# Optimization experiments

Hardware: AMD Instinct MI355X
Metric: run time of the kernel (lower is better)

The kernel has to match this reference:

```python
import jax, jax.numpy as jnp
import numpy as np

WS = 7  # window_size
EPS = 1e-5


def _ln(x, w, b):
    mu = jnp.mean(x, axis=-1, keepdims=True)
    var = jnp.mean((x - mu) ** 2, axis=-1, keepdims=True)
    return (x - mu) / jnp.sqrt(var + EPS) * w + b


def _mamba(xw, A, Bm, Cm):
    # xw: (N, T, C). h_t = x_t @ B + h_{t-1} @ A ; out = h @ C
    xB = xw @ Bm                      # (N, T, C) precompute input projection
    xs = jnp.swapaxes(xB, 0, 1)       # (T, N, C)

    def step(h, xb):
        h = xb + h @ A
        return h, h

    h0 = jnp.zeros_like(xs[0])
    _, hs = jax.lax.scan(step, h0, xs)  # (T, N, C)
    h = jnp.swapaxes(hs, 0, 1)          # (N, T, C)
    return h @ Cm


def setup_inputs() -> dict:
    key = jax.random.key(0)
    ks = jax.random.split(key, 12)
    dim = 384
    hid = 4 * dim
    s = 1.0 / np.sqrt(dim)
    d = {}
    d["x"] = jax.random.normal(ks[0], (16, 56, 56, dim), jnp.float32)
    # recurrence matrices scaled for numerical stability over T=49 steps
    d["A"] = jax.random.normal(ks[1], (dim, dim), jnp.float32) * (1.0 / dim)
    d["Bm"] = jax.random.normal(ks[2], (dim, dim), jnp.float32) * s
    d["Cm"] = jax.random.normal(ks[3], (dim, dim), jnp.float32) * s
    d["ln1_w"] = jnp.ones((dim,), jnp.float32)
    d["ln1_b"] = jnp.zeros((dim,), jnp.float32)
    d["ln2_w"] = jnp.ones((dim,), jnp.float32)
    d["ln2_b"] = jnp.zeros((dim,), jnp.float32)
    d["W1"] = jax.random.normal(ks[4], (dim, hid), jnp.float32) * s
    d["b1"] = jnp.zeros((hid,), jnp.float32)
    d["W2"] = jax.random.normal(ks[5], (hid, dim), jnp.float32) * (1.0 / np.sqrt(hid))
    d["b2"] = jnp.zeros((dim,), jnp.float32)
    return d


def reference(x, A, Bm, Cm, ln1_w, ln1_b, ln2_w, ln2_b, W1, b1, W2, b2):
    Bn, H, W, C = x.shape
    ws = WS
    # window_partition: (B,H,W,C) -> (B*nH*nW, ws*ws, C)
    w = x.reshape(Bn, H // ws, ws, W // ws, ws, C)
    w = w.transpose(0, 1, 3, 2, 4, 5).reshape(-1, ws * ws, C)
    w = _ln(w, ln1_w, ln1_b)
    w = _mamba(w, A, Bm, Cm)
    # window_reverse
    xr = w.reshape(Bn, H // ws, W // ws, ws, ws, C)
    xr = xr.transpose(0, 1, 3, 2, 4, 5).reshape(Bn, H, W, C)
    # MLP with residual (exact GELU, matching torch default)
    y = _ln(xr, ln2_w, ln2_b)
    y = jax.nn.gelu(y @ W1 + b1, approximate=False) @ W2 + b2
    return xr + y
```

## Files before the change

### kernel.cpp

```cpp
#include <hip/hip_runtime.h>
#include <hip/hip_bf16.h>
#include <math.h>

#define CDIM 384
#define HIDDIM 1536
#define HW56 56
#define WS 7
#define T49 49
#define MTOK 50176
#define MH 25088
#define DPOW 5
#define KSCAN (DPOW * CDIM)

typedef __bf16 bf16x8 __attribute__((ext_vector_type(8)));
typedef __bf16 bf16x4 __attribute__((ext_vector_type(4)));
typedef __bf16 bf16x2 __attribute__((ext_vector_type(2)));
typedef float f32x4 __attribute__((ext_vector_type(4)));

typedef const __attribute__((address_space(1))) void gas_void;
typedef __attribute__((address_space(3))) void las_void;

__device__ __forceinline__ void async16(const void* g, void* l) {
    __builtin_amdgcn_global_load_lds((gas_void*)g, (las_void*)l, 16, 0, 0);
}

__device__ __forceinline__ float fast_rcp(float x) {
#if __has_builtin(__builtin_amdgcn_rcpf)
    return __builtin_amdgcn_rcpf(x);
#else
    return 1.f / x;
#endif
}

__device__ __forceinline__ float fast_gelu(float v) {
    const float t = v + 0.044715f * v * v * v;
    const float e = __expf(-1.5957691216057308f * t);
    return v * fast_rcp(1.f + e);
}



__global__ __launch_bounds__(256) void transpose_to_bf16(
    const float* __restrict__ src, __bf16* __restrict__ dst, int R, int C)
{
    __shared__ float tile[64][65];
    const int c0 = blockIdx.x * 64, r0 = blockIdx.y * 64;
#pragma unroll
    for (int p = 0; p < 16; p++) {
        const int idx = threadIdx.x + p * 256;
        const int rr = idx >> 6, cc = idx & 63;
        tile[cc][rr] = src[(size_t)(r0 + rr) * C + c0 + cc];
    }
    __syncthreads();
#pragma unroll
    for (int p = 0; p < 16; p++) {
        const int idx = threadIdx.x + p * 256;
        const int cc = idx >> 6, rr = idx & 63;
        dst[(size_t)(c0 + cc) * R + r0 + rr] = (__bf16)tile[cc][rr];
    }
}

struct GemmJob  { const float* A; const float* B; float* D; };
struct GemmJobs { GemmJob j[3]; };

__global__ __launch_bounds__(256) void multi_gemm(GemmJobs jobs)
{
    __shared__ float As[16][68];
    __shared__ float Bs[16][68];
    const int tx = threadIdx.x & 15, ty = threadIdx.x >> 4;
    const int m0 = blockIdx.x * 64, n0 = blockIdx.y * 64;
    const GemmJob job = jobs.j[blockIdx.z];
    const float* Ain = job.A;
    const float* Bmat = job.B;
    float acc[4][4] = {};

    for (int k0 = 0; k0 < CDIM; k0 += 16) {
#pragma unroll
        for (int l = 0; l < 4; l++) {
            const int idx = threadIdx.x + l * 256;
            const int am = idx >> 4, ak = idx & 15;
            As[ak][am] = Ain[(size_t)(m0 + am) * CDIM + (k0 + ak)];
            const int bk = idx >> 6, bn = idx & 63;
            Bs[bk][bn] = Bmat[(size_t)(k0 + bk) * CDIM + (n0 + bn)];
        }
        __syncthreads();
#pragma unroll
        for (int kk = 0; kk < 16; kk++) {
            const float4 a4 = *reinterpret_cast<const float4*>(&As[kk][ty * 4]);
            const float4 b4 = *reinterpret_cast<const float4*>(&Bs[kk][tx * 4]);
            const float a[4]  = {a4.x, a4.y, a4.z, a4.w};
            const float bv[4] = {b4.x, b4.y, b4.z, b4.w};
#pragma unroll
            for (int i = 0; i < 4; i++)
#pragma unroll
                for (int j = 0; j < 4; j++) acc[i][j] += a[i] * bv[j];
        }
        __syncthreads();
    }
#pragma unroll
    for (int i = 0; i < 4; i++)
#pragma unroll
        for (int j = 0; j < 4; j++)
            job.D[(size_t)(m0 + ty * 4 + i) * CDIM + n0 + tx * 4 + j] = acc[i][j];
}

__global__ __launch_bounds__(256) void mcat_gemm(
    const float* __restrict__ Am, const float* __restrict__ Bmat, __bf16* __restrict__ Out)
{
    __shared__ float As[16][68];
    __shared__ float Bs[16][68];
    const int tx = threadIdx.x & 15, ty = threadIdx.x >> 4;
    const int m0 = blockIdx.x * 64, n0 = blockIdx.y * 64;
    const float* Ain = Am + (size_t)blockIdx.z * (CDIM * CDIM);
    float acc[4][4] = {};

    for (int k0 = 0; k0 < CDIM; k0 += 16) {
#pragma unroll
        for (int l = 0; l < 4; l++) {
            const int idx = threadIdx.x + l * 256;
            const int am = idx >> 4, ak = idx & 15;
            As[ak][am] = Ain[(size_t)(m0 + am) * CDIM + (k0 + ak)];
            const int bk = idx >> 6, bn = idx & 63;
            Bs[bk][bn] = Bmat[(size_t)(k0 + bk) * CDIM + (n0 + bn)];
        }
        __syncthreads();
#pragma unroll
        for (int kk = 0; kk < 16; kk++) {
            const float4 a4 = *reinterpret_cast<const float4*>(&As[kk][ty * 4]);
            const float4 b4 = *reinterpret_cast<const float4*>(&Bs[kk][tx * 4]);
            const float a[4]  = {a4.x, a4.y, a4.z, a4.w};
            const float bv[4] = {b4.x, b4.y, b4.z, b4.w};
#pragma unroll
            for (int i = 0; i < 4; i++)
#pragma unroll
                for (int j = 0; j < 4; j++) acc[i][j] += a[i] * bv[j];
        }
        __syncthreads();
    }
#pragma unroll
    for (int i = 0; i < 4; i++)
#pragma unroll
        for (int j = 0; j < 4; j++) {
            const int n = n0 + tx * 4 + j, m = m0 + ty * 4 + i;
            Out[(size_t)n * KSCAN + blockIdx.z * CDIM + m] = (__bf16)acc[i][j];
        }
}

__global__ void zerofill(float* p) { p[threadIdx.x] = 0.f; }

__global__ __launch_bounds__(256) void ln1_win_kernel(
    const float* __restrict__ x,
    const float* __restrict__ w,
    const float* __restrict__ b,
    __bf16* __restrict__ out)
{
    const int row  = blockIdx.x * 4 + (threadIdx.x >> 6);
    const int lane = threadIdx.x & 63;
    const int n = row / T49, t = row - n * T49;
    const int bb = n >> 6, rem = n & 63, hw = rem >> 3, ww = rem & 7;
    const int pi = t / WS, pj = t - pi * WS;
    const size_t pix = (size_t)(bb * HW56 + hw * WS + pi) * HW56 + (ww * WS + pj);
    const float* xr = x + pix * CDIM;

    float2 v[3]; float s = 0.f;
#pragma unroll
    for (int k = 0; k < 3; k++) {
        v[k] = *(const float2*)&xr[lane * 2 + 128 * k];
        s += v[k].x + v[k].y;
    }
#pragma unroll
    for (int off = 32; off > 0; off >>= 1) s += __shfl_down(s, off);
    const float mu = __shfl(s, 0) * (1.f / CDIM);
    float vs = 0.f;
#pragma unroll
    for (int k = 0; k < 3; k++) {
        const float dx = v[k].x - mu, dy = v[k].y - mu;
        vs += dx * dx + dy * dy;
    }
#pragma unroll
    for (int off = 32; off > 0; off >>= 1) vs += __shfl_down(vs, off);
    const float rstd = rsqrtf(__shfl(vs, 0) * (1.f / CDIM) + 1e-5f);

    __bf16* o = out + (size_t)row * CDIM;
#pragma unroll
    for (int k = 0; k < 3; k++) {
        const int c = lane * 2 + 128 * k;
        const float2 wv = *(const float2*)&w[c];
        const float2 bv = *(const float2*)&b[c];
        bf16x2 o2;
        o2[0] = (__bf16)((v[k].x - mu) * rstd * wv.x + bv.x);
        o2[1] = (__bf16)((v[k].y - mu) * rstd * wv.y + bv.y);
        *(bf16x2*)&o[c] = o2;
    }
}

__global__ __launch_bounds__(256) void ln2_kernel(
    const float* __restrict__ xr,
    const float* __restrict__ w,
    const float* __restrict__ b,
    __bf16* __restrict__ out)
{
    const int row  = blockIdx.x * 4 + (threadIdx.x >> 6);
    const int lane = threadIdx.x & 63;
    const float* xrow = xr + (size_t)row * CDIM;
    float2 v[3]; float s = 0.f;
#pragma unroll
    for (int k = 0; k < 3; k++) {
        v[k] = *(const float2*)&xrow[lane * 2 + 128 * k];
        s += v[k].x + v[k].y;
    }
#pragma unroll
    for (int off = 32; off > 0; off >>= 1) s += __shfl_down(s, off);
    const float mu = __shfl(s, 0) * (1.f / CDIM);
    float vs = 0.f;
#pragma unroll
    for (int k = 0; k < 3; k++) {
        const float dx = v[k].x - mu, dy = v[k].y - mu;
        vs += dx * dx + dy * dy;
    }
#pragma unroll
    for (int off = 32; off > 0; off >>= 1) vs += __shfl_down(vs, off);
    const float rstd = rsqrtf(__shfl(vs, 0) * (1.f / CDIM) + 1e-5f);

    __bf16* o = out + (size_t)row * CDIM;
#pragma unroll
    for (int k = 0; k < 3; k++) {
        const int c = lane * 2 + 128 * k;
        const float2 wv = *(const float2*)&w[c];
        const float2 bv = *(const float2*)&b[c];
        bf16x2 o2;
        o2[0] = (__bf16)((v[k].x - mu) * rstd * wv.x + bv.x);
        o2[1] = (__bf16)((v[k].y - mu) * rstd * wv.y + bv.y);
        *(bf16x2*)&o[c] = o2;
    }
}

__global__ __launch_bounds__(256) void gemm_scan(
    const __bf16* __restrict__ X,
    const __bf16* __restrict__ Wt,
    const __bf16* __restrict__ zerob,
    float* __restrict__ Out)
{
    __shared__ __bf16 Xs[136 * 64];
    __shared__ __bf16 Ws[128 * 64];

    const int nwg = gridDim.x;
    const int q8 = nwg >> 3, r8 = nwg & 7;
    const int xcd = blockIdx.x & 7, lin = blockIdx.x >> 3;
    const int id = (xcd < r8 ? xcd * (q8 + 1) : r8 * (q8 + 1) + (xcd - r8) * q8) + lin;
    const int bx = id / 3, by = id - bx * 3;

    const int tid  = threadIdx.x;
    const int w    = tid >> 6;
    const int lane = tid & 63;
    const int quad = lane >> 4, l15 = lane & 15;
    const int wm = w & 1, wn = w >> 1;
    const int m0 = bx * 128;
    const int n0 = by * 128;
    const int srow8 = lane >> 3;
    const int scol  = ((lane & 7) ^ srow8) * 8;

    const bool head  = (m0 == 0);
    const bool tailb = (m0 + 132 > MTOK);

    int tpos[4];
#pragma unroll
    for (int s = 0; s < 4; s++) tpos[s] = (m0 + wm * 64 + s * 16 + l15) % T49;

    const __bf16* Wbase = Wt + (size_t)(n0 + w * 32 + srow8) * KSCAN + scol;
    const __bf16* Xbase = X + ((size_t)m0 + w * 32 + srow8) * CDIM + scol - 4 * CDIM;

    const bf16x8 zero8 = {};
    f32x4 acc[4][4] = {};

    for (int kb = 0; kb < CDIM; kb += 64) {
        for (int j = 0; j < DPOW; j++) {
            __syncthreads();
            if (j == 0) {
#pragma unroll
                for (int c = 0; c < 4; c++) {
                    const __bf16* src = Xbase + (size_t)(c * 8) * CDIM + kb;
                    if (head && w == 0 && c == 0 && srow8 < 4) src = zerob;
                    async16(src, &Xs[(w * 32 + c * 8) * 64]);
                }
                if (w == 0) {
                    const int tk = m0 + 124 + srow8;
                    const __bf16* src = X + (size_t)tk * CDIM + kb + scol;
                    if (tailb && tk >= MTOK) src = zerob;
                    async16(src, &Xs[128 * 64]);
                }
            }
#pragma unroll
            for (int c = 0; c < 4; c++) {
                async16(Wbase + (size_t)(c * 8) * KSCAN + j * CDIM + kb, &Ws[(w * 32 + c * 8) * 64]);
            }
            __syncthreads();
#pragma unroll
            for (int kh = 0; kh < 2; kh++) {
                bf16x8 a[4], b[4];
#pragma unroll
                for (int s = 0; s < 4; s++) {
                    const int xrow = wm * 64 + s * 16 + l15 + 4 - j;
                    const int apos = ((kh * 4 + quad) ^ (xrow & 7)) * 8;
                    const bf16x8 av = *(const bf16x8*)&Xs[xrow * 64 + apos];
                    a[s] = (tpos[s] >= j) ? av : zero8;
                    const int rb = wn * 64 + s * 16 + l15;
                    const int bpos = ((kh * 4 + quad) ^ (l15 & 7)) * 8;
                    b[s] = *(const bf16x8*)&Ws[rb * 64 + bpos];
                }
#pragma unroll
                for (int i = 0; i < 4; i++)
#pragma unroll
                    for (int jj = 0; jj < 4; jj++)
                        acc[i][jj] = __builtin_amdgcn_mfma_f32_16x16x32_bf16(b[jj], a[i], acc[i][jj], 0, 0, 0);
            }
        }
    }

#pragma unroll
    for (int i = 0; i < 4; i++) {
        const int gm = m0 + wm * 64 + i * 16 + l15;
        const int n = gm / T49, t = gm - n * T49;
        const int bb = n >> 6, rem = n & 63, hw = rem >> 3, ww = rem & 7;
        const int pi = t / WS, pj = t - pi * WS;
        const size_t orow = (size_t)(bb * HW56 + hw * WS + pi) * HW56 + (ww * WS + pj);
#pragma unroll
        for (int jj = 0; jj < 4; jj++) {
            const int gn0 = n0 + wn * 64 + jj * 16 + quad * 4;
            *(f32x4*)&Out[orow * CDIM + gn0] = acc[i][jj];
        }
    }
}

template <int EPI, int NY>
__global__ __launch_bounds__(256) void gemm_mfma(
    const __bf16* __restrict__ X,
    const __bf16* __restrict__ Wt,
    const float*  __restrict__ bias,
    const float*  resid,
    void* Out, const int K, const int Nout)
{
    __shared__ __bf16 Xs[2][128 * 64];
    __shared__ __bf16 Ws[2][128 * 64];

    const int nwg = gridDim.x;
    const int q8 = nwg >> 3, r8 = nwg & 7;
    const int xcd = blockIdx.x & 7, lin = blockIdx.x >> 3;
    const int id = (xcd < r8 ? xcd * (q8 + 1) : r8 * (q8 + 1) + (xcd - r8) * q8) + lin;
    const int bx = id / NY, by = id - bx * NY;

    const int tid  = threadIdx.x;
    const int w    = tid >> 6;
    const int lane = tid & 63;
    const int quad = lane >> 4, l15 = lane & 15;
    const int wm = w & 1, wn = w >> 1;
    const size_t m0 = (size_t)bx * 128;
    const int n0 = by * 128;
    const int srow = w * 32 + (lane >> 3);
    const int scol = (((lane & 7) ^ (lane >> 3)) * 8);

    f32x4 acc[4][4] = {};

    const __bf16* Xrow = X + (m0 + srow) * (size_t)K + scol;
    const __bf16* Wrow = Wt + ((size_t)(n0 + srow)) * K + scol;

    auto stage = [&](int p, int bufi) {
        const int k0 = p * 64;
#pragma unroll
        for (int c = 0; c < 4; c++) {
            async16(Xrow + (size_t)(c * 8) * K + k0, &Xs[bufi][(w * 32 + c * 8) * 64]);
            async16(Wrow + (size_t)(c * 8) * K + k0, &Ws[bufi][(w * 32 + c * 8) * 64]);
        }
    };

    const int NP = K >> 6;
    stage(0, 0);
    __syncthreads();

    for (int p = 0; p < NP; p++) {
        if (p + 1 < NP) stage(p + 1, (p + 1) & 1);
        const int cb = p & 1;
#pragma unroll
        for (int kk = 0; kk < 2; kk++) {
            bf16x8 a[4], b[4];
#pragma unroll
            for (int s = 0; s < 4; s++) {
                const int ra = wm * 64 + s * 16 + l15;
                const int rb = wn * 64 + s * 16 + l15;
                const int pos = ((kk * 4 + quad) ^ (l15 & 7)) * 8;
                a[s] = *(const bf16x8*)&Xs[cb][ra * 64 + pos];
                b[s] = *(const bf16x8*)&Ws[cb][rb * 64 + pos];
            }
#pragma unroll
            for (int i = 0; i < 4; i++)
#pragma unroll
                for (int j = 0; j < 4; j++)
                    acc[i][j] = __builtin_amdgcn_mfma_f32_16x16x32_bf16(b[j], a[i], acc[i][j], 0, 0, 0);
        }
        __syncthreads();
    }

#pragma unroll
    for (int i = 0; i < 4; i++) {
        const size_t gm = m0 + wm * 64 + i * 16 + l15;
#pragma unroll
        for (int j = 0; j < 4; j++) {
            const int gn0 = n0 + wn * 64 + j * 16 + quad * 4;
            const float4 bs = *(const float4*)&bias[gn0];
            if (EPI == 2) {
                bf16x4 h;
#pragma unroll
                for (int r = 0; r < 4; r++) {
                    const float v = acc[i][j][r] + (&bs.x)[r];
                    h[r] = (__bf16)fast_gelu(v);
                }
                *(bf16x4*)&((__bf16*)Out)[gm * (size_t)Nout + gn0] = h;
            } else {
                const float4 rs = *(const float4*)&resid[gm * CDIM + gn0];
                f32x4 o;
#pragma unroll
                for (int r = 0; r < 4; r++) o[r] = acc[i][j][r] + (&bs.x)[r] + (&rs.x)[r];
                *(f32x4*)&((float*)Out)[gm * CDIM + gn0] = o;
            }
        }
    }
}

extern "C" void kernel_launch(void* const* d_in, const int* in_sizes, int n_in,
                              void* d_out, int out_size, void* d_ws, size_t ws_size,
                              hipStream_t stream) {
    const float* x    = (const float*)d_in[0];
    const float* A    = (const float*)d_in[1];
    const float* Bm   = (const float*)d_in[2];
    const float* Cm   = (const float*)d_in[3];
    const float* ln1w = (const float*)d_in[4];
    const float* ln1b = (const float*)d_in[5];
    const float* ln2w = (const float*)d_in[6];
    const float* ln2b = (const float*)d_in[7];
    const float* W1   = (const float*)d_in[8];
    const float* b1   = (const float*)d_in[9];
    const float* W2   = (const float*)d_in[10];
    const float* b2   = (const float*)d_in[11];

    float* outf = (float*)d_out;

    char* ws = (char*)d_ws;
    __bf16* B1     = (__bf16*)ws;
    float*  P      = (float*) (ws + 38535168);
    float*  A2     = (float*) (ws + 38535168 + DPOW * 589824);
    __bf16* Mcat_t = (__bf16*)(ws + 38535168 + (DPOW + 1) * 589824);
    float*  zerob  = (float*) (ws + 38535168 + (DPOW + 1) * 589824 + KSCAN * 768);
    float*  A4     = (float*) (ws + 38535168 + (DPOW + 1) * 589824 + KSCAN * 768 + 4096);
    __bf16* Hid    = (__bf16*)ws;
    __bf16* B2     = (__bf16*)(ws + 77070336);
    __bf16* W1_t   = (__bf16*)(ws + 115605504);
    __bf16* W2_t   = (__bf16*)(ws + 116785152);

    hipMemcpyAsync(P, Bm, (size_t)CDIM * CDIM * 4, hipMemcpyDeviceToDevice, stream);
    zerofill<<<1, 128, 0, stream>>>(zerob);
    transpose_to_bf16<<<dim3(24, 6), 256, 0, stream>>>(W1, W1_t, 384, 1536);
    transpose_to_bf16<<<dim3(6, 24), 256, 0, stream>>>(W2, W2_t, 1536, 384);

    {
        GemmJobs j1;
        j1.j[0] = {A, A, A2};
        j1.j[1] = {Bm, A, P + 1 * CDIM * CDIM};
        j1.j[2] = {A, A, A2};
        multi_gemm<<<dim3(6, 6, 2), 256, 0, stream>>>(j1);
        GemmJobs j2;
        j2.j[0] = {A2, A2, A4};
        j2.j[1] = {P, A2, P + 2 * CDIM * CDIM};
        j2.j[2] = {P + 1 * CDIM * CDIM, A2, P + 3 * CDIM * CDIM};
        multi_gemm<<<dim3(6, 6, 3), 256, 0, stream>>>(j2);
        GemmJobs j3;
        j3.j[0] = {P, A4, P + 4 * CDIM * CDIM};
        j3.j[1] = j3.j[0];
        j3.j[2] = j3.j[0];
        multi_gemm<<<dim3(6, 6, 1), 256, 0, stream>>>(j3);
    }
    mcat_gemm<<<dim3(6, 6, DPOW), 256, 0, stream>>>(P, Cm, Mcat_t);

    ln1_win_kernel<<<MTOK / 4, 256, 0, stream>>>(x, ln1w, ln1b, B1);
    gemm_scan<<<dim3((MTOK / 128) * 3), 256, 0, stream>>>(B1, Mcat_t, (const __bf16*)zerob, outf);
    ln2_kernel<<<MTOK / 4, 256, 0, stream>>>(outf, ln2w, ln2b, B2);
    for (int h = 0; h < 2; h++) {
        const size_t off = (size_t)h * MH * CDIM;
        gemm_mfma<2, 12><<<dim3((MH / 128) * 12), 256, 0, stream>>>(B2 + off, W1_t, b1, nullptr, Hid, 384, 1536);
        gemm_mfma<3, 3><<<dim3((MH / 128) * 3), 256, 0, stream>>>(Hid, W2_t, b2, outf + off, outf + off, 1536, 384);
    }
}
```

Before: 587.2 us.

## Reassociate weight-power precompute and shrink MLP GEMM K-stage to 32

The small weight-precompute chain is reassociated: instead of computing A^4 and then Bm*A^4 before multiplying by Cm, it computes U2=A^2*Cm and forms the fifth block as P2*U2. This drops the memcpy and one serial multi_gemm launch, and mcat_gemm now takes per-slice A/B pointers. Separately, the MLP MFMA GEMM stages 32-wide K tiles instead of 64, with a new LDS swizzle. That halves shared memory per block to help occupancy, at the cost of twice as many pipeline iterations and barriers.

```diff
diff --git a/kernel.cpp b/kernel.cpp
--- a/kernel.cpp
+++ b/kernel.cpp
@@ -104,14 +104,16 @@
             job.D[(size_t)(m0 + ty * 4 + i) * CDIM + n0 + tx * 4 + j] = acc[i][j];
 }
 
-__global__ __launch_bounds__(256) void mcat_gemm(
-    const float* __restrict__ Am, const float* __restrict__ Bmat, __bf16* __restrict__ Out)
+struct McatJobs { const float* Aj[DPOW]; const float* Bj[DPOW]; };
+
+__global__ __launch_bounds__(256) void mcat_gemm(McatJobs jobs, __bf16* __restrict__ Out)
 {
     __shared__ float As[16][68];
     __shared__ float Bs[16][68];
     const int tx = threadIdx.x & 15, ty = threadIdx.x >> 4;
     const int m0 = blockIdx.x * 64, n0 = blockIdx.y * 64;
-    const float* Ain = Am + (size_t)blockIdx.z * (CDIM * CDIM);
+    const float* Ain  = jobs.Aj[blockIdx.z];
+    const float* Bmat = jobs.Bj[blockIdx.z];
     float acc[4][4] = {};
 
     for (int k0 = 0; k0 < CDIM; k0 += 16) {
@@ -340,8 +342,8 @@
     const float*  resid,
     void* Out, const int K, const int Nout)
 {
-    __shared__ __bf16 Xs[2][128 * 64];
-    __shared__ __bf16 Ws[2][128 * 64];
+    __shared__ __bf16 Xs[2][128 * 32];
+    __shared__ __bf16 Ws[2][128 * 32];
 
     const int nwg = gridDim.x;
     const int q8 = nwg >> 3, r8 = nwg & 7;
@@ -356,47 +358,44 @@
     const int wm = w & 1, wn = w >> 1;
     const size_t m0 = (size_t)bx * 128;
     const int n0 = by * 128;
-    const int srow = w * 32 + (lane >> 3);
-    const int scol = (((lane & 7) ^ (lane >> 3)) * 8);
+    const int srow4 = lane >> 2;
+    const int sc4   = lane & 3;
 
     f32x4 acc[4][4] = {};
 
-    const __bf16* Xrow = X + (m0 + srow) * (size_t)K + scol;
-    const __bf16* Wrow = Wt + ((size_t)(n0 + srow)) * K + scol;
-
     auto stage = [&](int p, int bufi) {
-        const int k0 = p * 64;
-#pragma unroll
-        for (int c = 0; c < 4; c++) {
-            async16(Xrow + (size_t)(c * 8) * K + k0, &Xs[bufi][(w * 32 + c * 8) * 64]);
-            async16(Wrow + (size_t)(c * 8) * K + k0, &Ws[bufi][(w * 32 + c * 8) * 64]);
+        const int k0 = p * 32;
+#pragma unroll
+        for (int c = 0; c < 2; c++) {
+            const int R  = w * 32 + c * 16 + srow4;
+            const int lc = ((sc4 ^ ((R >> 1) & 3)) * 8);
+            async16(X  + (m0 + R) * (size_t)K + k0 + lc, &Xs[bufi][(w * 32 + c * 16) * 32]);
+            async16(Wt + (size_t)(n0 + R) * K + k0 + lc, &Ws[bufi][(w * 32 + c * 16) * 32]);
         }
     };
 
-    const int NP = K >> 6;
+    const int NP = K >> 5;
     stage(0, 0);
     __syncthreads();
 
     for (int p = 0; p < NP; p++) {
         if (p + 1 < NP) stage(p + 1, (p + 1) & 1);
         const int cb = p & 1;
-#pragma unroll
-        for (int kk = 0; kk < 2; kk++) {
-            bf16x8 a[4], b[4];
-#pragma unroll
-            for (int s = 0; s < 4; s++) {
-                const int ra = wm * 64 + s * 16 + l15;
-                const int rb = wn * 64 + s * 16 + l15;
-                const int pos = ((kk * 4 + quad) ^ (l15 & 7)) * 8;
-                a[s] = *(const bf16x8*)&Xs[cb][ra * 64 + pos];
-                b[s] = *(const bf16x8*)&Ws[cb][rb * 64 + pos];
-            }
-#pragma unroll
-            for (int i = 0; i < 4; i++)
-#pragma unroll
-                for (int j = 0; j < 4; j++)
-                    acc[i][j] = __builtin_amdgcn_mfma_f32_16x16x32_bf16(b[j], a[i], acc[i][j], 0, 0, 0);
-        }
+        bf16x8 a[4], b[4];
+#pragma unroll
+        for (int s = 0; s < 4; s++) {
+            const int ra = wm * 64 + s * 16 + l15;
+            const int rb = wn * 64 + s * 16 + l15;
+            const int pa = (quad ^ ((ra >> 1) & 3)) * 8;
+            const int pb = (quad ^ ((rb >> 1) & 3)) * 8;
+            a[s] = *(const bf16x8*)&Xs[cb][ra * 32 + pa];
+            b[s] = *(const bf16x8*)&Ws[cb][rb * 32 + pb];
+        }
+#pragma unroll
+        for (int i = 0; i < 4; i++)
+#pragma unroll
+            for (int j = 0; j < 4; j++)
+                acc[i][j] = __builtin_amdgcn_mfma_f32_16x16x32_bf16(b[j], a[i], acc[i][j], 0, 0, 0);
         __syncthreads();
     }
 
@@ -450,35 +449,38 @@
     float*  A2     = (float*) (ws + 38535168 + DPOW * 589824);
     __bf16* Mcat_t = (__bf16*)(ws + 38535168 + (DPOW + 1) * 589824);
     float*  zerob  = (float*) (ws + 38535168 + (DPOW + 1) * 589824 + KSCAN * 768);
-    float*  A4     = (float*) (ws + 38535168 + (DPOW + 1) * 589824 + KSCAN * 768 + 4096);
+    float*  U2     = (float*) (ws + 38535168 + (DPOW + 1) * 589824 + KSCAN * 768 + 4096);
     __bf16* Hid    = (__bf16*)ws;
     __bf16* B2     = (__bf16*)(ws + 77070336);
     __bf16* W1_t   = (__bf16*)(ws + 115605504);
     __bf16* W2_t   = (__bf16*)(ws + 116785152);
 
-    hipMemcpyAsync(P, Bm, (size_t)CDIM * CDIM * 4, hipMemcpyDeviceToDevice, stream);
+    float* P1 = P + 1 * CDIM * CDIM;
+    float* P2 = P + 2 * CDIM * CDIM;
+    float* P3 = P + 3 * CDIM * CDIM;
+
     zerofill<<<1, 128, 0, stream>>>(zerob);
     transpose_to_bf16<<<dim3(24, 6), 256, 0, stream>>>(W1, W1_t, 384, 1536);
     transpose_to_bf16<<<dim3(6, 24), 256, 0, stream>>>(W2, W2_t, 1536, 384);
-
     {
         GemmJobs j1;
         j1.j[0] = {A, A, A2};
-        j1.j[1] = {Bm, A, P + 1 * CDIM * CDIM};
+        j1.j[1] = {Bm, A, P1};
         j1.j[2] = {A, A, A2};
         multi_gemm<<<dim3(6, 6, 2), 256, 0, stream>>>(j1);
         GemmJobs j2;
-        j2.j[0] = {A2, A2, A4};
-        j2.j[1] = {P, A2, P + 2 * CDIM * CDIM};
-        j2.j[2] = {P + 1 * CDIM * CDIM, A2, P + 3 * CDIM * CDIM};
+        j2.j[0] = {A2, Cm, U2};
+        j2.j[1] = {Bm, A2, P2};
+        j2.j[2] = {P1, A2, P3};
         multi_gemm<<<dim3(6, 6, 3), 256, 0, stream>>>(j2);
-        GemmJobs j3;
-        j3.j[0] = {P, A4, P + 4 * CDIM * CDIM};
-        j3.j[1] = j3.j[0];
-        j3.j[2] = j3.j[0];
-        multi_gemm<<<dim3(6, 6, 1), 256, 0, stream>>>(j3);
-    }
-    mcat_gemm<<<dim3(6, 6, DPOW), 256, 0, stream>>>(P, Cm, Mcat_t);
+        McatJobs mj;
+        mj.Aj[0] = Bm; mj.Bj[0] = Cm;
+        mj.Aj[1] = P1; mj.Bj[1] = Cm;
+        mj.Aj[2] = P2; mj.Bj[2] = Cm;
+        mj.Aj[3] = P3; mj.Bj[3] = Cm;
+        mj.Aj[4] = P2; mj.Bj[4] = U2;
+        mcat_gemm<<<dim3(6, 6, DPOW), 256, 0, stream>>>(mj, Mcat_t);
+    }
 
     ln1_win_kernel<<<MTOK / 4, 256, 0, stream>>>(x, ln1w, ln1b, B1);
     gemm_scan<<<dim3((MTOK / 128) * 3), 256, 0, stream>>>(B1, Mcat_t, (const __bf16*)zerob, outf);
```

Result: faster. 569.5 us (-3.0%).
